# Kernel optimization log

Hardware: AMD Instinct MI355X
Metric: run time of the kernel (lower is better)

Reference implementation:

```python
import jax, jax.numpy as jnp
import numpy as np

ALPHA = 1.702  # sigmoid-GLU scale
LIMIT = 7.0    # clamp limit
TOP_K = 2      # num_experts_per_tok


def setup_inputs() -> dict:
    key = jax.random.key(0)
    ks = jax.random.split(key, 4)
    B, S, H, E, I = 2, 1024, 1024, 8, 2048
    return {
        "hidden_states": jax.random.normal(ks[0], (B, S, H), jnp.float32),
        "router_weight": jax.random.normal(ks[1], (E, H), jnp.float32),
        "router_bias": jnp.zeros((E,), jnp.float32),
        "gate_up_proj": jax.random.normal(ks[2], (E, H, 2 * I), jnp.float32) * 0.02,
        "gate_up_bias": jnp.zeros((E, 2 * I), jnp.float32),
        "down_proj": jax.random.normal(ks[3], (E, I, H), jnp.float32) * 0.02,
        "down_bias": jnp.zeros((E, H), jnp.float32),
    }


def reference(hidden_states, router_weight, router_bias, gate_up_proj,
              gate_up_bias, down_proj, down_bias):
    B, S, H = hidden_states.shape
    E, _, two_I = gate_up_proj.shape
    I = two_I // 2

    flat = hidden_states.reshape(B * S, H)  # [T, H]

    # Router: softmax + top-k
    logits = flat @ router_weight.T + router_bias            # [T, E]
    scores = jax.nn.softmax(logits, axis=-1)
    topk_w, topk_idx = jax.lax.top_k(scores, TOP_K)          # [T, K]

    # Dense per-expert gated FFN (einsum 'abmh,ehn->abemn' computes all experts
    # on all tokens; the reshape/permute dance is a mathematical no-op).
    gu = jnp.einsum('th,ehn->ten', flat, gate_up_proj) + gate_up_bias  # [T, E, 2I]
    gate = jnp.minimum(gu[..., :I], LIMIT)
    up = jnp.clip(gu[..., I:], -LIMIT, LIMIT)
    glu = gate * jax.nn.sigmoid(gate * ALPHA)
    act = (up + 1.0) * glu                                   # [T, E, I]

    down = jnp.einsum('tei,eih->teh', act, down_proj) + down_bias  # [T, E, H]

    # Combine: gather each token's top-k expert outputs, weighted sum.
    gathered = jnp.take_along_axis(down, topk_idx[:, :, None], axis=1)  # [T, K, H]
    out = (gathered * topk_w[:, :, None]).sum(axis=1)        # [T, H]
    return out.reshape(B, S, H)
```

## Files before the change

### kernel.cpp

```cpp
#include <hip/hip_runtime.h>
#include <math.h>

#define TT 2048
#define HH 1024
#define EE 8
#define II 2048
#define N1 4096
#define ALPHA 1.702f
#define LIMIT 7.0f

typedef __attribute__((ext_vector_type(8))) short short8;
typedef __attribute__((ext_vector_type(4))) float floatx4;
typedef __attribute__((ext_vector_type(4))) unsigned int uintx4;

__device__ __forceinline__ short f2bf(float f) {
  union { float f; unsigned u; } v; v.f = f;
  unsigned r = (v.u + 0x7fffu + ((v.u >> 16) & 1u)) >> 16;
  return (short)r;
}
__device__ __forceinline__ unsigned cvt2(float lo, float hi) {
  unsigned r;
  asm("v_cvt_pk_bf16_f32 %0, %1, %2" : "=v"(r) : "v"(lo), "v"(hi));
  return r;
}
__device__ __forceinline__ void gload16(const void* g, void* l) {
  __builtin_amdgcn_global_load_lds(
      (const __attribute__((address_space(1))) unsigned int*)g,
      (__attribute__((address_space(3))) unsigned int*)l, 16, 0, 0);
}

__global__ __launch_bounds__(256) void transpose_bf16(
    const float* __restrict__ src, unsigned short* __restrict__ dst,
    const int K, const int N) {
  const int e = blockIdx.z;
  const int n0 = blockIdx.x * 64, k0 = blockIdx.y * 64;
  __shared__ float tile[64][68];
  const float* s = src + (size_t)e * K * N;
  unsigned short* d = dst + (size_t)e * N * K;
  const int t = threadIdx.x;
  const int nq = t & 15, kr = t >> 4;
#pragma unroll
  for (int r = 0; r < 4; r++) {
    const int k = r * 16 + kr;
    const float4 v = *(const float4*)(s + (size_t)(k0 + k) * N + n0 + nq * 4);
    tile[k][nq * 4 + 0] = v.x; tile[k][nq * 4 + 1] = v.y;
    tile[k][nq * 4 + 2] = v.z; tile[k][nq * 4 + 3] = v.w;
  }
  __syncthreads();
  const int n = t >> 2, ks = (t & 3) * 16;
  unsigned short* orow = d + (size_t)(n0 + n) * K + k0 + ks;
  uintx4 w0, w1;
#pragma unroll
  for (int m = 0; m < 4; m++)
    w0[m] = cvt2(tile[ks + 2 * m][n], tile[ks + 2 * m + 1][n]);
#pragma unroll
  for (int m = 0; m < 4; m++)
    w1[m] = cvt2(tile[ks + 8 + 2 * m][n], tile[ks + 9 + 2 * m][n]);
  *(uintx4*)orow = w0;
  *(uintx4*)(orow + 8) = w1;
}

__global__ __launch_bounds__(256) void router_kernel(
    const float* __restrict__ x, const float* __restrict__ rw,
    const float* __restrict__ rb, float* __restrict__ topk_w,
    int* __restrict__ counts, int* __restrict__ rows,
    unsigned short* __restrict__ xb) {
  const int t = blockIdx.x;
  const float* xr = x + (size_t)t * HH;
  const int lane = threadIdx.x & 63;
  const int wave = threadIdx.x >> 6;
  float xv[16];
#pragma unroll
  for (int i = 0; i < 16; i++) xv[i] = xr[lane + i * 64];
  __shared__ float logits[EE];
#pragma unroll
  for (int ee = 0; ee < 2; ee++) {
    const int e = wave * 2 + ee;
    const float* wr = rw + (size_t)e * HH;
    float s = 0.f;
#pragma unroll
    for (int i = 0; i < 16; i++) s += xv[i] * wr[lane + i * 64];
#pragma unroll
    for (int off = 32; off > 0; off >>= 1) s += __shfl_down(s, off, 64);
    if (lane == 0) logits[e] = s + rb[e];
  }
  if (wave == 0) {
    unsigned short* xo = xb + (size_t)t * HH;
#pragma unroll
    for (int i = 0; i < 16; i++) xo[lane + i * 64] = (unsigned short)f2bf(xv[i]);
  }
  __syncthreads();
  if (threadIdx.x == 0) {
    float l[EE], sc[EE];
    float mx = -3.4e38f;
    for (int i = 0; i < EE; i++) { l[i] = logits[i]; mx = fmaxf(mx, l[i]); }
    float sum = 0.f;
    for (int i = 0; i < EE; i++) { sc[i] = expf(l[i] - mx); sum += sc[i]; }
    const float inv = 1.f / sum;
    int i0 = 0;
    for (int i = 1; i < EE; i++) if (sc[i] > sc[i0]) i0 = i;
    int i1 = (i0 == 0) ? 1 : 0;
    for (int i = 0; i < EE; i++) if (i != i0 && sc[i] > sc[i1]) i1 = i;
    topk_w[t * 2 + 0] = sc[i0] * inv;
    topk_w[t * 2 + 1] = sc[i1] * inv;
    const int s0 = atomicAdd(&counts[i0], 1);
    rows[i0 * TT + s0] = t * 2 + 0;
    const int s1 = atomicAdd(&counts[i1], 1);
    rows[i1 * TT + s1] = t * 2 + 1;
  }
}

__global__ __launch_bounds__(256, 2) void gemm_gu(
    const unsigned short* __restrict__ xb, const unsigned short* __restrict__ gupt,
    const float* __restrict__ gub, const int* __restrict__ counts,
    const int* __restrict__ rows, unsigned short* __restrict__ act) {
  const int e = blockIdx.z, mtile = blockIdx.y, ntile = blockIdx.x;
  const int count = counts[e];
  if (mtile * 128 >= count) return;
  const int* rl = rows + e * TT + mtile * 128;
  __shared__ __align__(16) char smem[65536];
  unsigned short* As = (unsigned short*)smem;
  unsigned short* Bs = (unsigned short*)(smem + 32768);
  float* glds = (float*)smem;
  const int tid = threadIdx.x;
  const int lane = tid & 63, wave = tid >> 6;
  const int wm = (wave & 1) << 6, wn = (wave >> 1) << 6;
  const int quad = lane >> 4, r16 = lane & 15;

  const int lrow = lane >> 2, lko = (lane & 3) * 8;
  const int q0 = wave * 2, q1 = q0 + 1;
  const int row0 = q0 * 16 + lrow, row1 = q1 * 16 + lrow;
  const int last = count - 1 - mtile * 128;
  const int cr0 = row0 <= last ? row0 : last;
  const int cr1 = row1 <= last ? row1 : last;
  const unsigned short* pA0 = xb + (size_t)(rl[cr0] >> 1) * HH + lko;
  const unsigned short* pA1 = xb + (size_t)(rl[cr1] >> 1) * HH + lko;
  const int bn0 = (row0 < 64) ? (ntile * 64 + row0) : (II + ntile * 64 + row0 - 64);
  const int bn1 = (row1 < 64) ? (ntile * 64 + row1) : (II + ntile * 64 + row1 - 64);
  const unsigned short* pB0 = gupt + (size_t)e * N1 * HH + (size_t)bn0 * HH + lko;
  const unsigned short* pB1 = gupt + (size_t)e * N1 * HH + (size_t)bn1 * HH + lko;
  unsigned short* dA0 = As + q0 * 512;
  unsigned short* dA1 = As + q1 * 512;
  unsigned short* dB0 = Bs + q0 * 512;
  unsigned short* dB1 = Bs + q1 * 512;

  floatx4 acc[4][4] = {};
  const int NTK = HH / 32;

#define STAGE(B, kk) do { \
    const int ko_ = (kk) * 32; \
    gload16(pA0 + ko_, dA0 + (B) * 4096); \
    gload16(pA1 + ko_, dA1 + (B) * 4096); \
    gload16(pB0 + ko_, dB0 + (B) * 4096); \
    gload16(pB1 + ko_, dB1 + (B) * 4096); \
  } while (0)

#define PHASE(B) do { \
    asm volatile("s_waitcnt vmcnt(12)" ::: "memory"); \
    __builtin_amdgcn_s_barrier(); \
    short8 af[4], bf4[4]; \
    _Pragma("unroll") for (int i = 0; i < 4; i++) \
      af[i] = *(const short8*)(As + (B) * 4096 + (wm + i * 16 + r16) * 32 + quad * 8); \
    _Pragma("unroll") for (int j = 0; j < 4; j++) \
      bf4[j] = *(const short8*)(Bs + (B) * 4096 + (wn + j * 16 + r16) * 32 + quad * 8); \
    asm volatile("s_waitcnt lgkmcnt(0)" ::: "memory"); \
    __builtin_amdgcn_sched_barrier(0); \
    __builtin_amdgcn_s_barrier(); \
    { const int ks_ = kn < NTK ? kn : NTK - 1; kn++; STAGE(B, ks_); } \
    __builtin_amdgcn_sched_barrier(0); \
    __builtin_amdgcn_s_setprio(1); \
    _Pragma("unroll") for (int i = 0; i < 4; i++) \
      _Pragma("unroll") for (int j = 0; j < 4; j++) \
        acc[i][j] = __builtin_amdgcn_mfma_f32_16x16x32_bf16(af[i], bf4[j], acc[i][j], 0, 0, 0); \
    __builtin_amdgcn_s_setprio(0); \
  } while (0)

  STAGE(0, 0);
  STAGE(1, 1);
  STAGE(2, 2);
  STAGE(3, 3);
  int kn = 4;
#pragma unroll 1
  for (int t = 0; t < NTK; t += 4) {
    PHASE(0);
    PHASE(1);
    PHASE(2);
    PHASE(3);
  }
  asm volatile("s_waitcnt vmcnt(0)" ::: "memory");
  __builtin_amdgcn_s_barrier();

  const int colbase = ntile * 64;
  if (wn == 0) {
#pragma unroll
    for (int j = 0; j < 4; j++) {
      const int c = j * 16 + r16;
      const float gb = gub[e * N1 + colbase + c];
#pragma unroll
      for (int i = 0; i < 4; i++)
#pragma unroll
        for (int reg = 0; reg < 4; reg++) {
          const int rr = wm + i * 16 + quad * 4 + reg;
          float g = acc[i][j][reg] + gb;
          g = fminf(g, LIMIT);
          glds[rr * 65 + c] = g / (1.f + expf(-g * ALPHA));
        }
    }
  }
  __builtin_amdgcn_s_barrier();
  if (wn == 64) {
#pragma unroll
    for (int j = 0; j < 4; j++) {
      const int c = j * 16 + r16;
      const float ub = gub[e * N1 + II + colbase + c];
#pragma unroll
      for (int i = 0; i < 4; i++)
#pragma unroll
        for (int reg = 0; reg < 4; reg++) {
          const int rr = wm + i * 16 + quad * 4 + reg;
          if (mtile * 128 + rr < count) {
            float u = acc[i][j][reg] + ub;
            u = fminf(fmaxf(u, -LIMIT), LIMIT);
            const float glu = glds[rr * 65 + c];
            act[(size_t)rl[rr] * II + colbase + c] = (unsigned short)f2bf((u + 1.f) * glu);
          }
        }
    }
  }
#undef STAGE
#undef PHASE
}

__global__ __launch_bounds__(256, 2) void gemm_down(
    const unsigned short* __restrict__ act, const unsigned short* __restrict__ dpt,
    const float* __restrict__ db, const int* __restrict__ counts,
    const int* __restrict__ rows, const float* __restrict__ tw,
    float* __restrict__ out) {
  const int e = blockIdx.z >> 1, kc = blockIdx.z & 1;
  const int mtile = blockIdx.y, ntile = blockIdx.x;
  const int count = counts[e];
  if (mtile * 128 >= count) return;
  const int kb = kc * (II / 2);
  const int* rl = rows + e * TT + mtile * 128;
  __shared__ __align__(16) char smem[65536];
  unsigned short* As = (unsigned short*)smem;
  unsigned short* Bs = (unsigned short*)(smem + 32768);
  const int tid = threadIdx.x;
  const int lane = tid & 63, wave = tid >> 6;
  const int wm = (wave & 1) << 6, wn = (wave >> 1) << 6;
  const int quad = lane >> 4, r16 = lane & 15;

  const int lrow = lane >> 2, lko = (lane & 3) * 8;
  const int q0 = wave * 2, q1 = q0 + 1;
  const int row0 = q0 * 16 + lrow, row1 = q1 * 16 + lrow;
  const int last = count - 1 - mtile * 128;
  const int cr0 = row0 <= last ? row0 : last;
  const int cr1 = row1 <= last ? row1 : last;
  const unsigned short* pA0 = act + (size_t)rl[cr0] * II + kb + lko;
  const unsigned short* pA1 = act + (size_t)rl[cr1] * II + kb + lko;
  const unsigned short* pB0 = dpt + (size_t)e * HH * II + (size_t)(ntile * 128 + row0) * II + kb + lko;
  const unsigned short* pB1 = dpt + (size_t)e * HH * II + (size_t)(ntile * 128 + row1) * II + kb + lko;
  unsigned short* dA0 = As + q0 * 512;
  unsigned short* dA1 = As + q1 * 512;
  unsigned short* dB0 = Bs + q0 * 512;
  unsigned short* dB1 = Bs + q1 * 512;

  floatx4 acc[4][4] = {};
  const int NTK = (II / 2) / 32;

#define STAGE(B, kk) do { \
    const int ko_ = (kk) * 32; \
    gload16(pA0 + ko_, dA0 + (B) * 4096); \
    gload16(pA1 + ko_, dA1 + (B) * 4096); \
    gload16(pB0 + ko_, dB0 + (B) * 4096); \
    gload16(pB1 + ko_, dB1 + (B) * 4096); \
  } while (0)

#define PHASE(B) do { \
    asm volatile("s_waitcnt vmcnt(12)" ::: "memory"); \
    __builtin_amdgcn_s_barrier(); \
    short8 af[4], bf4[4]; \
    _Pragma("unroll") for (int i = 0; i < 4; i++) \
      af[i] = *(const short8*)(As + (B) * 4096 + (wm + i * 16 + r16) * 32 + quad * 8); \
    _Pragma("unroll") for (int j = 0; j < 4; j++) \
      bf4[j] = *(const short8*)(Bs + (B) * 4096 + (wn + j * 16 + r16) * 32 + quad * 8); \
    asm volatile("s_waitcnt lgkmcnt(0)" ::: "memory"); \
    __builtin_amdgcn_sched_barrier(0); \
    __builtin_amdgcn_s_barrier(); \
    { const int ks_ = kn < NTK ? kn : NTK - 1; kn++; STAGE(B, ks_); } \
    __builtin_amdgcn_sched_barrier(0); \
    __builtin_amdgcn_s_setprio(1); \
    _Pragma("unroll") for (int i = 0; i < 4; i++) \
      _Pragma("unroll") for (int j = 0; j < 4; j++) \
        acc[i][j] = __builtin_amdgcn_mfma_f32_16x16x32_bf16(af[i], bf4[j], acc[i][j], 0, 0, 0); \
    __builtin_amdgcn_s_setprio(0); \
  } while (0)

  STAGE(0, 0);
  STAGE(1, 1);
  STAGE(2, 2);
  STAGE(3, 3);
  int kn = 4;
#pragma unroll 1
  for (int t = 0; t < NTK; t += 4) {
    PHASE(0);
    PHASE(1);
    PHASE(2);
    PHASE(3);
  }
  asm volatile("s_waitcnt vmcnt(0)" ::: "memory");
  __builtin_amdgcn_s_barrier();

#pragma unroll
  for (int i = 0; i < 4; i++) {
#pragma unroll
    for (int reg = 0; reg < 4; reg++) {
      const int rr = wm + i * 16 + quad * 4 + reg;
      if (mtile * 128 + rr < count) {
        const int ent = rl[rr];
        const float w = tw[ent];
        float* orow = out + (size_t)(ent >> 1) * HH + ntile * 128;
#pragma unroll
        for (int j = 0; j < 4; j++) {
          const int c = wn + j * 16 + r16;
          float v = acc[i][j][reg];
          if (kc == 0) v += db[e * HH + ntile * 128 + c];
          atomicAdd(&orow[c], w * v);
        }
      }
    }
  }
#undef STAGE
#undef PHASE
}

extern "C" void kernel_launch(void* const* d_in, const int* in_sizes, int n_in,
                              void* d_out, int out_size, void* d_ws, size_t ws_size,
                              hipStream_t stream) {
  const float* x   = (const float*)d_in[0];
  const float* rw  = (const float*)d_in[1];
  const float* rb  = (const float*)d_in[2];
  const float* gup = (const float*)d_in[3];
  const float* gub = (const float*)d_in[4];
  const float* dp  = (const float*)d_in[5];
  const float* db  = (const float*)d_in[6];
  float* out = (float*)d_out;

  char* ws = (char*)d_ws;
  float* topk_w   = (float*)(ws + 0);
  int*   counts   = (int*)(ws + 16384);
  int*   rows     = (int*)(ws + 16640);
  unsigned short* xb   = (unsigned short*)(ws + 131072);
  unsigned short* gupt = (unsigned short*)(ws + 4325376);
  unsigned short* dpt  = (unsigned short*)(ws + 71434240);
  unsigned short* act  = (unsigned short*)(ws + 104988672);

  hipMemsetAsync(counts, 0, 64, stream);
  hipMemsetAsync(out, 0, (size_t)TT * HH * 4, stream);
  router_kernel<<<TT, 256, 0, stream>>>(x, rw, rb, topk_w, counts, rows, xb);
  transpose_bf16<<<dim3(N1 / 64, HH / 64, EE), 256, 0, stream>>>(gup, gupt, HH, N1);
  transpose_bf16<<<dim3(HH / 64, II / 64, EE), 256, 0, stream>>>(dp, dpt, II, HH);
  gemm_gu<<<dim3(II / 64, TT / 128, EE), 256, 0, stream>>>(xb, gupt, gub, counts, rows, act);
  gemm_down<<<dim3(HH / 128, TT / 128, EE * 2), 256, 0, stream>>>(act, dpt, db, counts, rows, topk_w, out);
}
```

Measured before the change: 484.1 us.

## Merge transposes, fold memsets into kernels, halve LDS stages, swizzle GEMM grids

Folds the two weight transposes into one launch and moves the counts and output zeroing into the transpose and router kernels, removing two memsets and a launch. Both grouped GEMMs drop from four to two LDS pipeline stages, which halves shared memory so four blocks per CU can be resident instead of two. The GEMM grids become 1D with an XCD-style swizzle so that blocks sharing an expert's weights land near each other. The shallower prefetch exposes more memory latency per block, which the extra occupancy is meant to hide.

```diff
diff --git a/kernel.cpp b/kernel.cpp
--- a/kernel.cpp
+++ b/kernel.cpp
@@ -29,11 +29,23 @@
       (__attribute__((address_space(3))) unsigned int*)l, 16, 0, 0);
 }
 
-__global__ __launch_bounds__(256) void transpose_bf16(
-    const float* __restrict__ src, unsigned short* __restrict__ dst,
-    const int K, const int N) {
-  const int e = blockIdx.z;
-  const int n0 = blockIdx.x * 64, k0 = blockIdx.y * 64;
+__global__ __launch_bounds__(256) void transpose_all(
+    const float* __restrict__ gup, const float* __restrict__ dp,
+    unsigned short* __restrict__ gupt, unsigned short* __restrict__ dpt,
+    int* __restrict__ counts) {
+  const int id = blockIdx.x;
+  if (id == 0 && threadIdx.x < 16) counts[threadIdx.x] = 0;
+  const float* src;
+  unsigned short* dst;
+  int K, N, n0, k0, e;
+  if (id < 8192) {
+    src = gup; dst = gupt; K = HH; N = N1;
+    n0 = (id & 63) * 64; k0 = ((id >> 6) & 15) * 64; e = id >> 10;
+  } else {
+    const int id2 = id - 8192;
+    src = dp; dst = dpt; K = II; N = HH;
+    n0 = (id2 & 15) * 64; k0 = ((id2 >> 4) & 31) * 64; e = id2 >> 9;
+  }
   __shared__ float tile[64][68];
   const float* s = src + (size_t)e * K * N;
   unsigned short* d = dst + (size_t)e * N * K;
@@ -64,11 +76,13 @@
     const float* __restrict__ x, const float* __restrict__ rw,
     const float* __restrict__ rb, float* __restrict__ topk_w,
     int* __restrict__ counts, int* __restrict__ rows,
-    unsigned short* __restrict__ xb) {
+    unsigned short* __restrict__ xb, float* __restrict__ out) {
   const int t = blockIdx.x;
   const float* xr = x + (size_t)t * HH;
   const int lane = threadIdx.x & 63;
   const int wave = threadIdx.x >> 6;
+  const float4 z = {0.f, 0.f, 0.f, 0.f};
+  ((float4*)(out + (size_t)t * HH))[threadIdx.x] = z;
   float xv[16];
 #pragma unroll
   for (int i = 0; i < 16; i++) xv[i] = xr[lane + i * 64];
@@ -110,17 +124,20 @@
   }
 }
 
-__global__ __launch_bounds__(256, 2) void gemm_gu(
+__global__ __launch_bounds__(256, 4) void gemm_gu(
     const unsigned short* __restrict__ xb, const unsigned short* __restrict__ gupt,
     const float* __restrict__ gub, const int* __restrict__ counts,
     const int* __restrict__ rows, unsigned short* __restrict__ act) {
-  const int e = blockIdx.z, mtile = blockIdx.y, ntile = blockIdx.x;
+  const int swz = (blockIdx.x & 7) * (4096 / 8) + (blockIdx.x >> 3);
+  const int mtile = swz & 15;
+  const int ntile = (swz >> 4) & 31;
+  const int e = swz >> 9;
   const int count = counts[e];
   if (mtile * 128 >= count) return;
   const int* rl = rows + e * TT + mtile * 128;
-  __shared__ __align__(16) char smem[65536];
+  __shared__ __align__(16) char smem[33280];
   unsigned short* As = (unsigned short*)smem;
-  unsigned short* Bs = (unsigned short*)(smem + 32768);
+  unsigned short* Bs = (unsigned short*)(smem + 16384);
   float* glds = (float*)smem;
   const int tid = threadIdx.x;
   const int lane = tid & 63, wave = tid >> 6;
@@ -156,7 +173,7 @@
   } while (0)
 
 #define PHASE(B) do { \
-    asm volatile("s_waitcnt vmcnt(12)" ::: "memory"); \
+    asm volatile("s_waitcnt vmcnt(4)" ::: "memory"); \
     __builtin_amdgcn_s_barrier(); \
     short8 af[4], bf4[4]; \
     _Pragma("unroll") for (int i = 0; i < 4; i++) \
@@ -177,15 +194,11 @@
 
   STAGE(0, 0);
   STAGE(1, 1);
-  STAGE(2, 2);
-  STAGE(3, 3);
-  int kn = 4;
+  int kn = 2;
 #pragma unroll 1
-  for (int t = 0; t < NTK; t += 4) {
+  for (int t = 0; t < NTK; t += 2) {
     PHASE(0);
     PHASE(1);
-    PHASE(2);
-    PHASE(3);
   }
   asm volatile("s_waitcnt vmcnt(0)" ::: "memory");
   __builtin_amdgcn_s_barrier();
@@ -231,20 +244,22 @@
 #undef PHASE
 }
 
-__global__ __launch_bounds__(256, 2) void gemm_down(
+__global__ __launch_bounds__(256, 4) void gemm_down(
     const unsigned short* __restrict__ act, const unsigned short* __restrict__ dpt,
     const float* __restrict__ db, const int* __restrict__ counts,
     const int* __restrict__ rows, const float* __restrict__ tw,
     float* __restrict__ out) {
-  const int e = blockIdx.z >> 1, kc = blockIdx.z & 1;
-  const int mtile = blockIdx.y, ntile = blockIdx.x;
+  const int swz = (blockIdx.x & 7) * (2048 / 8) + (blockIdx.x >> 3);
+  const int mtile = swz & 15;
+  const int ntile = (swz >> 4) & 7;
+  const int e = swz >> 8, kc = (swz >> 7) & 1;
   const int count = counts[e];
   if (mtile * 128 >= count) return;
   const int kb = kc * (II / 2);
   const int* rl = rows + e * TT + mtile * 128;
-  __shared__ __align__(16) char smem[65536];
+  __shared__ __align__(16) char smem[32768];
   unsigned short* As = (unsigned short*)smem;
-  unsigned short* Bs = (unsigned short*)(smem + 32768);
+  unsigned short* Bs = (unsigned short*)(smem + 16384);
   const int tid = threadIdx.x;
   const int lane = tid & 63, wave = tid >> 6;
   const int wm = (wave & 1) << 6, wn = (wave >> 1) << 6;
@@ -277,7 +292,7 @@
   } while (0)
 
 #define PHASE(B) do { \
-    asm volatile("s_waitcnt vmcnt(12)" ::: "memory"); \
+    asm volatile("s_waitcnt vmcnt(4)" ::: "memory"); \
     __builtin_amdgcn_s_barrier(); \
     short8 af[4], bf4[4]; \
     _Pragma("unroll") for (int i = 0; i < 4; i++) \
@@ -298,15 +313,11 @@
 
   STAGE(0, 0);
   STAGE(1, 1);
-  STAGE(2, 2);
-  STAGE(3, 3);
-  int kn = 4;
+  int kn = 2;
 #pragma unroll 1
-  for (int t = 0; t < NTK; t += 4) {
+  for (int t = 0; t < NTK; t += 2) {
     PHASE(0);
     PHASE(1);
-    PHASE(2);
-    PHASE(3);
   }
   asm volatile("s_waitcnt vmcnt(0)" ::: "memory");
   __builtin_amdgcn_s_barrier();
@@ -355,11 +366,8 @@
   unsigned short* dpt  = (unsigned short*)(ws + 71434240);
   unsigned short* act  = (unsigned short*)(ws + 104988672);
 
-  hipMemsetAsync(counts, 0, 64, stream);
-  hipMemsetAsync(out, 0, (size_t)TT * HH * 4, stream);
-  router_kernel<<<TT, 256, 0, stream>>>(x, rw, rb, topk_w, counts, rows, xb);
-  transpose_bf16<<<dim3(N1 / 64, HH / 64, EE), 256, 0, stream>>>(gup, gupt, HH, N1);
-  transpose_bf16<<<dim3(HH / 64, II / 64, EE), 256, 0, stream>>>(dp, dpt, II, HH);
-  gemm_gu<<<dim3(II / 64, TT / 128, EE), 256, 0, stream>>>(xb, gupt, gub, counts, rows, act);
-  gemm_down<<<dim3(HH / 128, TT / 128, EE * 2), 256, 0, stream>>>(act, dpt, db, counts, rows, topk_w, out);
-}
+  transpose_all<<<12288, 256, 0, stream>>>(gup, dp, gupt, dpt, counts);
+  router_kernel<<<TT, 256, 0, stream>>>(x, rw, rb, topk_w, counts, rows, xb, out);
+  gemm_gu<<<4096, 256, 0, stream>>>(xb, gupt, gub, counts, rows, act);
+  gemm_down<<<2048, 256, 0, stream>>>(act, dpt, db, counts, rows, topk_w, out);
+}
```

Result: no change. 477.1 us (-1.4%).
